# Performance work log

Hardware: AMD Instinct MI355X
Metric: run time of the kernel (lower is better)

The kernel has to match this reference:

```python
import jax, jax.numpy as jnp
import numpy as np

B, N, M, K, D, DO = 4, 32768, 8192, 16, 128, 128


def setup_inputs() -> dict:
    key = jax.random.key(0)
    ks = jax.random.split(key, 8)
    return dict(
        xyz=jax.random.normal(ks[0], (B, N, 3), jnp.float32),
        x=jax.random.normal(ks[1], (B, D, N), jnp.float32),
        xyz_center=jax.random.normal(ks[2], (B, M, 3), jnp.float32),
        idx=jax.random.randint(ks[3], (B, M, K), 0, N, jnp.int32),
        alpha=jnp.ones((1,), jnp.float32),
        beta=jnp.ones((1,), jnp.float32),
        norm_radius=jnp.ones((1,), jnp.float32),
        w1=jax.random.normal(ks[4], (K, 3), jnp.float32) * 0.1,
        g1=jnp.ones((K,), jnp.float32),
        b1=jnp.zeros((K,), jnp.float32),
        w2=jax.random.normal(ks[5], (K, 2 * K), jnp.float32) * 0.1,
        g2=jnp.ones((K,), jnp.float32),
        b2=jnp.zeros((K,), jnp.float32),
        w3=jax.random.normal(ks[6], (K, 2 * K), jnp.float32) * 0.1,
        cv_w=jax.random.normal(ks[7], (DO, D, K), jnp.float32) * 0.02,
    )


def _inorm(t, g, b, eps=1e-5):
    # InstanceNorm2d: normalize each (batch, channel) plane over spatial dims (m, k)
    mu = t.mean(axis=(2, 3), keepdims=True)
    var = t.var(axis=(2, 3), keepdims=True)
    return (t - mu) * jax.lax.rsqrt(var + eps) * g[None, :, None, None] + b[None, :, None, None]


def reference(xyz, x, xyz_center, idx, alpha, beta, norm_radius, w1, g1, b1, w2, g2, b2, w3, cv_w):
    k = idx.shape[-1]
    gather = jax.vmap(lambda pts, i: pts[i])  # per-batch gather
    xyz_group = gather(xyz, idx)                      # b m k 3
    x_group = gather(jnp.swapaxes(x, 1, 2), idx)      # b m k d

    pts = xyz_group - xyz_center[:, :, None, :]       # b m k 3
    # dist computed on detached pts (torch .detach())
    dist = jnp.sqrt(jnp.sum(jnp.square(jax.lax.stop_gradient(pts)), -1))  # b m k
    mean_radius = dist.max(-1).mean()
    nr = norm_radius * 0.9 + mean_radius * 0.1        # EMA-updated radius (non-trainable)
    pts = pts / nr

    dw = jax.nn.sigmoid(-alpha * dist + beta)         # b m k
    s = dw.sum(-1, keepdims=True)
    s = s + (s == 0).astype(dw.dtype) + 1e-6
    dw = dw / s * k
    dw4 = dw[:, None, :, :]                           # b 1 m k

    ptsT = jnp.transpose(pts, (0, 3, 1, 2))           # b 3 m k
    mat = jax.nn.relu(_inorm(jnp.einsum('bcmk,oc->bomk', ptsT, w1), g1, b1))
    mp1 = jnp.broadcast_to((mat * dw4).max(-1, keepdims=True), mat.shape)
    mat = jax.nn.relu(_inorm(jnp.einsum('bcmk,oc->bomk', jnp.concatenate([mat, mp1], 1), w2), g2, b2))
    mp2 = jnp.broadcast_to((mat * dw4).max(-1, keepdims=True), mat.shape)
    mat = jax.nn.relu(jnp.einsum('bcmk,oc->bomk', jnp.concatenate([mat, mp2], 1), w3)) * dw4

    out = jnp.einsum('bmkd,bjmk->bdmj', x_group, mat)  # b d m k
    out = jnp.einsum('bdmj,odj->bom', out, cv_w)
    return out
```

## Files before the change

kernel.cpp:

```cpp
#include <hip/hip_runtime.h>
#include <hip/hip_bf16.h>

#define BB 4
#define NN 32768
#define MM 8192
#define KK 16
#define DD 128
#define DOUT 128
#define TT 2048

typedef unsigned short ushortT;
typedef unsigned int uintT;
typedef __attribute__((ext_vector_type(8))) short short8;
typedef __attribute__((ext_vector_type(4))) float f32x4;
typedef __attribute__((ext_vector_type(2))) float f32x2;

__device__ __forceinline__ ushortT f2bf(float f) {
  union { float f; uintT u; } v; v.f = f;
  uintT u = v.u;
  return (ushortT)((u + 0x7FFFu + ((u >> 16) & 1u)) >> 16);
}

#define ST_MAXD 0
#define ST_E1 16
#define ST_A1 160
#define ST_B1 224
#define ST_E2 288
#define ST_A2 416
#define ST_B2 480

__global__ __launch_bounds__(256) void kxT(const float* __restrict__ x, ushortT* __restrict__ xTb) {
  __shared__ float tile[32][33];
  const int b = blockIdx.z;
  const int n0 = blockIdx.x * 32, d0 = blockIdx.y * 32;
  const int tx = threadIdx.x, ty = threadIdx.y;
  const float* xp = x + (size_t)b * DD * NN;
  #pragma unroll
  for (int i = 0; i < 4; i++)
    tile[ty + i * 8][tx] = xp[(size_t)(d0 + ty + i * 8) * NN + n0 + tx];
  __syncthreads();
  ushortT* op = xTb + (size_t)b * NN * DD;
  #pragma unroll
  for (int i = 0; i < 4; i++)
    op[(size_t)(n0 + ty + i * 8) * DD + d0 + tx] = f2bf(tile[tx][ty + i * 8]);
}

__global__ __launch_bounds__(256) void kWb(const float* __restrict__ cw, ushortT* __restrict__ wb) {
  const int i = blockIdx.x * 256 + threadIdx.x;
  wb[i] = f2bf(cw[i]);
}

__global__ __launch_bounds__(256) void kpassA(const float* __restrict__ xyz,
    const float* __restrict__ xyzc, const int* __restrict__ idx,
    const float* __restrict__ w1, float* __restrict__ st, float4* __restrict__ pts4) {
  const int b = blockIdx.y;
  const int tid = threadIdx.x;
  const int mloc = tid >> 4, k = tid & 15;
  const int m = blockIdx.x * 16 + mloc;
  const int gi = (b * MM + m) * KK + k;
  const int n = idx[gi];
  const float cx = xyzc[(b * MM + m) * 3 + 0];
  const float cy = xyzc[(b * MM + m) * 3 + 1];
  const float cz = xyzc[(b * MM + m) * 3 + 2];
  const float* p = xyz + ((size_t)b * NN + n) * 3;
  const float px = p[0] - cx, py = p[1] - cy, pz = p[2] - cz;
  const float dist = sqrtf(px * px + py * py + pz * pz);
  pts4[gi] = (float4){px, py, pz, dist};
  float maxd = dist;
  maxd = fmaxf(maxd, __shfl_xor(maxd, 1));
  maxd = fmaxf(maxd, __shfl_xor(maxd, 2));
  maxd = fmaxf(maxd, __shfl_xor(maxd, 4));
  maxd = fmaxf(maxd, __shfl_xor(maxd, 8));
  __shared__ float red[16];
  __shared__ float wred[4][32];
  if (k == 0) red[mloc] = maxd;
  float vs[16], vq[16];
  #pragma unroll
  for (int o = 0; o < 16; o++) {
    float e = px * w1[3 * o] + py * w1[3 * o + 1] + pz * w1[3 * o + 2];
    vs[o] = e; vq[o] = e * e;
  }
  #pragma unroll
  for (int s = 1; s < 64; s <<= 1) {
    #pragma unroll
    for (int o = 0; o < 16; o++) {
      vs[o] += __shfl_xor(vs[o], s);
      vq[o] += __shfl_xor(vq[o], s);
    }
  }
  const int wv = tid >> 6, lane = tid & 63;
  if (lane == 0) {
    #pragma unroll
    for (int o = 0; o < 16; o++) { wred[wv][o] = vs[o]; wred[wv][16 + o] = vq[o]; }
  }
  __syncthreads();
  if (tid < 32) {
    float a = wred[0][tid] + wred[1][tid] + wred[2][tid] + wred[3][tid];
    atomicAdd(&st[ST_E1 + b * 32 + tid], a);
  }
  if (tid == 0) {
    float s = 0.f;
    #pragma unroll
    for (int i = 0; i < 16; i++) s += red[i];
    atomicAdd(&st[ST_MAXD], s);
  }
}

__global__ void kS1(const float* __restrict__ nrad, const float* __restrict__ g1,
                    const float* __restrict__ b1, float* __restrict__ st) {
  const int tid = threadIdx.x;
  if (tid >= 64) return;
  const float meanrad = st[ST_MAXD] / (float)(BB * MM);
  const float nr = nrad[0] * 0.9f + meanrad * 0.1f;
  const int b = tid >> 4, o = tid & 15;
  const float cnt = (float)(MM * KK);
  const float sum = st[ST_E1 + b * 32 + o];
  const float sq  = st[ST_E1 + b * 32 + 16 + o];
  const float mu = sum / cnt;
  float var = sq / cnt - mu * mu; var = fmaxf(var, 0.f);
  const float invs = rsqrtf(var + 1e-5f * nr * nr);
  const float a = invs * g1[o];
  st[ST_A1 + b * 16 + o] = a;
  st[ST_B1 + b * 16 + o] = b1[o] - mu * a;
}

__global__ __launch_bounds__(256) void kpassB(const float4* __restrict__ pts4,
    const float* __restrict__ alpha, const float* __restrict__ beta,
    const float* __restrict__ w1, const float* __restrict__ w2,
    float* __restrict__ st) {
  const int b = blockIdx.y;
  const int tid = threadIdx.x;
  __shared__ float wred[4][32];
  const int gi = b * MM * KK + blockIdx.x * 256 + tid;
  const float4 p4 = pts4[gi];
  const float px = p4.x, py = p4.y, pz = p4.z, dist = p4.w;
  float dwv = 1.f / (1.f + expf(alpha[0] * dist - beta[0]));
  float s = dwv;
  s += __shfl_xor(s, 1); s += __shfl_xor(s, 2); s += __shfl_xor(s, 4); s += __shfl_xor(s, 8);
  s = s + (s == 0.f ? 1.f : 0.f) + 1e-6f;
  dwv = dwv / s * 16.f;
  f32x2 v1[16];
  #pragma unroll
  for (int o = 0; o < 16; o++) {
    float e = px * w1[3 * o] + py * w1[3 * o + 1] + pz * w1[3 * o + 2];
    float v = e * st[ST_A1 + b * 16 + o] + st[ST_B1 + b * 16 + o];
    v = fmaxf(v, 0.f);
    float t = v * dwv;
    t = fmaxf(t, __shfl_xor(t, 1)); t = fmaxf(t, __shfl_xor(t, 2));
    t = fmaxf(t, __shfl_xor(t, 4)); t = fmaxf(t, __shfl_xor(t, 8));
    if (o & 1) { v1[o >> 1].y = v; v1[8 + (o >> 1)].y = t; }
    else       { v1[o >> 1].x = v; v1[8 + (o >> 1)].x = t; }
  }
  float vs[16], vq[16];
  #pragma unroll
  for (int o = 0; o < 16; o++) {
    f32x2 acc = {0.f, 0.f};
    #pragma unroll
    for (int cp = 0; cp < 16; cp++) {
      const f32x2 wv = *(const f32x2*)(w2 + o * 32 + 2 * cp);
      acc += v1[cp] * wv;
    }
    const float e = acc.x + acc.y;
    vs[o] = e; vq[o] = e * e;
  }
  #pragma unroll
  for (int s2 = 1; s2 < 64; s2 <<= 1) {
    #pragma unroll
    for (int o = 0; o < 16; o++) {
      vs[o] += __shfl_xor(vs[o], s2);
      vq[o] += __shfl_xor(vq[o], s2);
    }
  }
  const int wv = tid >> 6, lane = tid & 63;
  if (lane == 0) {
    #pragma unroll
    for (int o = 0; o < 16; o++) { wred[wv][o] = vs[o]; wred[wv][16 + o] = vq[o]; }
  }
  __syncthreads();
  if (tid < 32) {
    float a = wred[0][tid] + wred[1][tid] + wred[2][tid] + wred[3][tid];
    atomicAdd(&st[ST_E2 + b * 32 + tid], a);
  }
}

__global__ void kS2(const float* __restrict__ g2, const float* __restrict__ b2,
                    float* __restrict__ st) {
  const int tid = threadIdx.x;
  if (tid >= 64) return;
  const int b = tid >> 4, o = tid & 15;
  const float cnt = (float)(MM * KK);
  const float sum = st[ST_E2 + b * 32 + o];
  const float sq  = st[ST_E2 + b * 32 + 16 + o];
  const float mu = sum / cnt;
  float var = sq / cnt - mu * mu; var = fmaxf(var, 0.f);
  const float invs = rsqrtf(var + 1e-5f);
  const float a = invs * g2[o];
  st[ST_A2 + b * 16 + o] = a;
  st[ST_B2 + b * 16 + o] = b2[o] - mu * a;
}

__global__ __launch_bounds__(256, 6) void kMat3(const float* __restrict__ xyz,
    const float* __restrict__ xyzc, const int* __restrict__ idx,
    const float* __restrict__ alpha, const float* __restrict__ beta,
    const float* __restrict__ w1, const float* __restrict__ w2,
    const float* __restrict__ w3, const float* __restrict__ st,
    float* __restrict__ mat3g) {
  const int b = blockIdx.y;
  const int tid = threadIdx.x;
  const int mloc = tid >> 4, k1 = tid & 15;
  const int m = blockIdx.x * 16 + mloc;
  const int gi = (b * MM + m) * KK + k1;
  const int n = idx[gi];
  const float cx = xyzc[(b * MM + m) * 3 + 0];
  const float cy = xyzc[(b * MM + m) * 3 + 1];
  const float cz = xyzc[(b * MM + m) * 3 + 2];
  const float* p = xyz + ((size_t)b * NN + n) * 3;
  const float px = p[0] - cx, py = p[1] - cy, pz = p[2] - cz;
  const float dist = sqrtf(px * px + py * py + pz * pz);
  float dwv = 1.f / (1.f + expf(alpha[0] * dist - beta[0]));
  {
    float s = dwv;
    s += __shfl_xor(s, 1); s += __shfl_xor(s, 2); s += __shfl_xor(s, 4); s += __shfl_xor(s, 8);
    s = s + (s == 0.f ? 1.f : 0.f) + 1e-6f;
    dwv = dwv / s * 16.f;
  }
  f32x2 v1[16];
  #pragma unroll
  for (int o = 0; o < 16; o++) {
    float e = px * w1[3 * o] + py * w1[3 * o + 1] + pz * w1[3 * o + 2];
    float v = e * st[ST_A1 + b * 16 + o] + st[ST_B1 + b * 16 + o];
    v = fmaxf(v, 0.f);
    float t = v * dwv;
    t = fmaxf(t, __shfl_xor(t, 1)); t = fmaxf(t, __shfl_xor(t, 2));
    t = fmaxf(t, __shfl_xor(t, 4)); t = fmaxf(t, __shfl_xor(t, 8));
    if (o & 1) { v1[o >> 1].y = v; v1[8 + (o >> 1)].y = t; }
    else       { v1[o >> 1].x = v; v1[8 + (o >> 1)].x = t; }
  }
  float in2[16];
  #pragma unroll
  for (int o = 0; o < 16; o++) {
    f32x2 acc = {0.f, 0.f};
    #pragma unroll
    for (int cp = 0; cp < 16; cp++) {
      const f32x2 wv = *(const f32x2*)(w2 + o * 32 + 2 * cp);
      acc += v1[cp] * wv;
    }
    float v = (acc.x + acc.y) * st[ST_A2 + b * 16 + o] + st[ST_B2 + b * 16 + o];
    in2[o] = fmaxf(v, 0.f);
  }
  f32x2 v2[16];
  #pragma unroll
  for (int o = 0; o < 16; o++) {
    float t = in2[o] * dwv;
    t = fmaxf(t, __shfl_xor(t, 1)); t = fmaxf(t, __shfl_xor(t, 2));
    t = fmaxf(t, __shfl_xor(t, 4)); t = fmaxf(t, __shfl_xor(t, 8));
    if (o & 1) { v2[o >> 1].y = in2[o]; v2[8 + (o >> 1)].y = t; }
    else       { v2[o >> 1].x = in2[o]; v2[8 + (o >> 1)].x = t; }
  }
  float m3v[16];
  #pragma unroll
  for (int j = 0; j < 16; j++) {
    f32x2 acc = {0.f, 0.f};
    #pragma unroll
    for (int cp = 0; cp < 16; cp++) {
      const f32x2 wv = *(const f32x2*)(w3 + j * 32 + 2 * cp);
      acc += v2[cp] * wv;
    }
    m3v[j] = fmaxf(acc.x + acc.y, 0.f) * dwv;
  }
  const int swz1 = (k1 ^ (k1 >> 2)) & 3;
  float* m3w = mat3g + (((size_t)b * MM + blockIdx.x * 16) << 8) + tid * 16;
  #pragma unroll
  for (int q = 0; q < 4; q++)
    *(f32x4*)(m3w + ((q ^ swz1) << 2)) =
        (f32x4){m3v[4 * q], m3v[4 * q + 1], m3v[4 * q + 2], m3v[4 * q + 3]};
}

__global__ __launch_bounds__(512, 4) void kF2(const int* __restrict__ idx,
    const float* __restrict__ mat3g, const ushortT* __restrict__ xTb,
    ushortT* __restrict__ Aout) {
  __shared__ float mat3s[32 * 256];
  const int b = blockIdx.y;
  const int tid = threadIdx.x;
  const int m0 = blockIdx.x * 32;

  const int wid = __builtin_amdgcn_readfirstlane(tid >> 6);
  const int lane = tid & 63;
  const int jh = lane >> 5;
  const int dq = lane & 31;
  const int d0 = dq * 4;
  const int jq0 = jh * 2;
  const ushortT* xb = xTb + (size_t)b * NN * DD + d0;

  uint2 xA[16], xB[16];

#define PREF(dst, gg) do {                                                 \
    const int* ib = idx + (((b * MM + m0 + (gg) * 8 + wid)) << 4);         \
    _Pragma("unroll")                                                      \
    for (int k = 0; k < 16; k++) {                                         \
      const uintT nn = (uintT)ib[k];                                       \
      (dst)[k] = *(const uint2*)(xb + ((size_t)nn << 7));                  \
    }                                                                      \
  } while (0)

  PREF(xA, 0);

  {
    const float* src = mat3g + (((size_t)b * MM + m0) << 8) + tid * 16;
    float* dst = &mat3s[tid * 16];
    #pragma unroll
    for (int q = 0; q < 4; q++)
      *(f32x4*)(dst + q * 4) = *(const f32x4*)(src + q * 4);
  }
  __syncthreads();

#define COMP(src, gg) do {                                                 \
    const int ml = (gg) * 8 + wid;                                         \
    const float* m3base = &mat3s[ml * 256];                                \
    f32x2 a2[4][4];                                                        \
    _Pragma("unroll")                                                      \
    for (int d = 0; d < 4; d++)                                            \
      _Pragma("unroll")                                                    \
      for (int c = 0; c < 4; c++) a2[d][c] = (f32x2){0.f, 0.f};            \
    _Pragma("unroll")                                                      \
    for (int k = 0; k < 16; k++) {                                         \
      const int sw = (k ^ (k >> 2)) & 3;                                   \
      const uint2 xv = (src)[k];                                           \
      const f32x4 mq0 = *(const f32x4*)(m3base + k * 16 + ((jq0 ^ sw) << 2));        \
      const f32x4 mq1 = *(const f32x4*)(m3base + k * 16 + (((jq0 + 1) ^ sw) << 2));  \
      float xs[4];                                                         \
      xs[0] = __uint_as_float(xv.x << 16);                                 \
      xs[1] = __uint_as_float(xv.x & 0xFFFF0000u);                         \
      xs[2] = __uint_as_float(xv.y << 16);                                 \
      xs[3] = __uint_as_float(xv.y & 0xFFFF0000u);                         \
      f32x2 mp[4];                                                         \
      mp[0] = mq0.lo; mp[1] = mq0.hi;                                      \
      mp[2] = mq1.lo; mp[3] = mq1.hi;                                      \
      _Pragma("unroll")                                                    \
      for (int d = 0; d < 4; d++) {                                        \
        const float xd = xs[d];                                            \
        _Pragma("unroll")                                                  \
        for (int c = 0; c < 4; c++)                                        \
          a2[d][c] += mp[c] * xd;                                          \
      }                                                                    \
    }                                                                      \
    ushortT* aop = Aout + ((size_t)b * MM + m0 + ml) * TT + d0 * 16 + jh * 8;  \
    _Pragma("unroll")                                                      \
    for (int d = 0; d < 4; d++) {                                          \
      uintT u[4];                                                          \
      _Pragma("unroll")                                                    \
      for (int c = 0; c < 4; c++)                                          \
        u[c] = (uintT)f2bf(a2[d][c].x) | ((uintT)f2bf(a2[d][c].y) << 16);  \
      *(uint4*)(aop + d * 16) = (uint4){u[0], u[1], u[2], u[3]};           \
    }                                                                      \
  } while (0)

  PREF(xB, 1);
  COMP(xA, 0);
  PREF(xA, 2);
  COMP(xB, 1);
  PREF(xB, 3);
  COMP(xA, 2);
  COMP(xB, 3);

#undef PREF
#undef COMP
}

__global__ __launch_bounds__(512) void kgemm(const ushortT* __restrict__ Wb,
                                             const ushortT* __restrict__ Aout,
                                             float* __restrict__ out) {
  __shared__ ushortT At[128 * 40];
  __shared__ ushortT Bt[128 * 40];
  const int b = blockIdx.y;
  const int m0 = blockIdx.x * 128;
  const int tid = threadIdx.x;
  const int w = tid >> 6, l = tid & 63;
  const int ow = (w >> 2) * 64, mw = (w & 3) * 32;
  const int fr = l & 15, fg = l >> 4;
  f32x4 acc[4][2];
  #pragma unroll
  for (int i = 0; i < 4; i++)
    #pragma unroll
    for (int j = 0; j < 2; j++)
      acc[i][j] = (f32x4){0.f, 0.f, 0.f, 0.f};
  const int srow = tid >> 2, sk = (tid & 3) * 8;
  const ushortT* wp = Wb + srow * TT + sk;
  const ushortT* ap = Aout + ((size_t)b * MM + m0 + srow) * TT + sk;
  for (int k0 = 0; k0 < TT; k0 += 32) {
    uint4 wv = *(const uint4*)(wp + k0);
    uint4 av = *(const uint4*)(ap + k0);
    *(uint4*)&At[srow * 40 + sk] = wv;
    *(uint4*)&Bt[srow * 40 + sk] = av;
    __syncthreads();
    short8 a[4], bfrag[2];
    #pragma unroll
    for (int i = 0; i < 4; i++) a[i] = *(short8*)&At[(ow + i * 16 + fr) * 40 + fg * 8];
    #pragma unroll
    for (int j = 0; j < 2; j++) bfrag[j] = *(short8*)&Bt[(mw + j * 16 + fr) * 40 + fg * 8];
    #pragma unroll
    for (int i = 0; i < 4; i++)
      #pragma unroll
      for (int j = 0; j < 2; j++)
        acc[i][j] = __builtin_amdgcn_mfma_f32_16x16x32_bf16(a[i], bfrag[j], acc[i][j], 0, 0, 0);
    __syncthreads();
  }
  #pragma unroll
  for (int i = 0; i < 4; i++)
    #pragma unroll
    for (int j = 0; j < 2; j++)
      #pragma unroll
      for (int r = 0; r < 4; r++) {
        const int o = ow + i * 16 + fg * 4 + r;
        const int m = m0 + mw + j * 16 + fr;
        out[((size_t)b * DOUT + o) * MM + m] = acc[i][j][r];
      }
}

#define XTB_OFF 0
#define PTS_OFF 33554432
#define MAT3_OFF 33554432
#define AOUT_OFF 67108864
#define WB_OFF 201326592
#define ST_OFF 201850880

extern "C" void kernel_launch(void* const* d_in, const int* in_sizes, int n_in,
                              void* d_out, int out_size, void* d_ws, size_t ws_size,
                              hipStream_t stream) {
  const float* xyz  = (const float*)d_in[0];
  const float* x    = (const float*)d_in[1];
  const float* xyzc = (const float*)d_in[2];
  const int*   idx  = (const int*)d_in[3];
  const float* alpha = (const float*)d_in[4];
  const float* beta  = (const float*)d_in[5];
  const float* nrad  = (const float*)d_in[6];
  const float* w1 = (const float*)d_in[7];
  const float* g1 = (const float*)d_in[8];
  const float* b1 = (const float*)d_in[9];
  const float* w2 = (const float*)d_in[10];
  const float* g2 = (const float*)d_in[11];
  const float* b2 = (const float*)d_in[12];
  const float* w3 = (const float*)d_in[13];
  const float* cvw = (const float*)d_in[14];
  char* ws = (char*)d_ws;
  ushortT* xTb  = (ushortT*)(ws + XTB_OFF);
  float4*  pts4 = (float4*)(ws + PTS_OFF);
  float*   mat3g = (float*)(ws + MAT3_OFF);
  ushortT* Aout = (ushortT*)(ws + AOUT_OFF);
  ushortT* Wb   = (ushortT*)(ws + WB_OFF);
  float*   st   = (float*)(ws + ST_OFF);
  float* out = (float*)d_out;

  hipMemsetAsync(st, 0, 4096, stream);
  kxT<<<dim3(NN / 32, DD / 32, BB), dim3(32, 8), 0, stream>>>(x, xTb);
  kWb<<<dim3(DOUT * TT / 256), 256, 0, stream>>>(cvw, Wb);
  kpassA<<<dim3(MM / 16, BB), 256, 0, stream>>>(xyz, xyzc, idx, w1, st, pts4);
  kS1<<<1, 64, 0, stream>>>(nrad, g1, b1, st);
  kpassB<<<dim3(MM / 16, BB), 256, 0, stream>>>(pts4, alpha, beta, w1, w2, st);
  kS2<<<1, 64, 0, stream>>>(g2, b2, st);
  kMat3<<<dim3(MM / 16, BB), 256, 0, stream>>>(xyz, xyzc, idx, alpha, beta, w1, w2, w3, st, mat3g);
  kF2<<<dim3(MM / 32, BB), 512, 0, stream>>>(idx, mat3g, xTb, Aout);
  kgemm<<<dim3(MM / 128, BB), 512, 0, stream>>>(Wb, Aout, out);
}
```

Before: 222.7 us.

## Remap kF2 lanes so each half-wave computes all 16 outputs of one point

In kF2 each half-wave now handles a separate center point and computes all 16 j outputs, where before the two half-waves split the j outputs of a single point. Each gathered x row is therefore loaded once per point instead of twice, which halves the gather traffic and cuts the four prefetch/compute stages to two. The shared-memory staging of mat3 switches to coalesced strided f32x4 copies. In exchange there are twice as many accumulators per thread, and launch bounds drop from 4 to 3 waves, which lowers occupancy.

```diff
diff --git a/kernel.cpp b/kernel.cpp
--- a/kernel.cpp
+++ b/kernel.cpp
@@ -276,7 +276,7 @@
         (f32x4){m3v[4 * q], m3v[4 * q + 1], m3v[4 * q + 2], m3v[4 * q + 3]};
 }
 
-__global__ __launch_bounds__(512, 4) void kF2(const int* __restrict__ idx,
+__global__ __launch_bounds__(512, 3) void kF2(const int* __restrict__ idx,
     const float* __restrict__ mat3g, const ushortT* __restrict__ xTb,
     ushortT* __restrict__ Aout) {
   __shared__ float mat3s[32 * 256];
@@ -286,82 +286,83 @@
 
   const int wid = __builtin_amdgcn_readfirstlane(tid >> 6);
   const int lane = tid & 63;
-  const int jh = lane >> 5;
+  const int mh = lane >> 5;
   const int dq = lane & 31;
   const int d0 = dq * 4;
-  const int jq0 = jh * 2;
   const ushortT* xb = xTb + (size_t)b * NN * DD + d0;
 
   uint2 xA[16], xB[16];
 
 #define PREF(dst, gg) do {                                                 \
-    const int* ib = idx + (((b * MM + m0 + (gg) * 8 + wid)) << 4);         \
+    const int* ib0 = idx + ((b * MM + m0 + (gg) * 16 + wid * 2) << 4);     \
+    const int* ib1 = ib0 + 16;                                             \
     _Pragma("unroll")                                                      \
-    for (int k = 0; k < 16; k++) {                                         \
-      const uintT nn = (uintT)ib[k];                                       \
-      (dst)[k] = *(const uint2*)(xb + ((size_t)nn << 7));                  \
+    for (int t = 0; t < 16; t++) {                                         \
+      const int ke = ib0[t], ko = ib1[t];                                  \
+      const uintT nn = (uintT)(mh ? ko : ke);                              \
+      (dst)[t] = *(const uint2*)(xb + ((size_t)nn << 7));                  \
     }                                                                      \
   } while (0)
 
   PREF(xA, 0);
 
   {
-    const float* src = mat3g + (((size_t)b * MM + m0) << 8) + tid * 16;
-    float* dst = &mat3s[tid * 16];
-    #pragma unroll
-    for (int q = 0; q < 4; q++)
-      *(f32x4*)(dst + q * 4) = *(const f32x4*)(src + q * 4);
+    const f32x4* src = (const f32x4*)(mat3g + (((size_t)b * MM + m0) << 8));
+    f32x4* dst = (f32x4*)mat3s;
+    #pragma unroll
+    for (int i = 0; i < 4; i++)
+      dst[tid + i * 512] = src[tid + i * 512];
   }
   __syncthreads();
 
 #define COMP(src, gg) do {                                                 \
-    const int ml = (gg) * 8 + wid;                                         \
-    const float* m3base = &mat3s[ml * 256];                                \
-    f32x2 a2[4][4];                                                        \
+    const float* m3base = &mat3s[((gg) * 16 + wid * 2 + mh) * 256];        \
+    f32x2 a2[4][8];                                                        \
     _Pragma("unroll")                                                      \
     for (int d = 0; d < 4; d++)                                            \
       _Pragma("unroll")                                                    \
-      for (int c = 0; c < 4; c++) a2[d][c] = (f32x2){0.f, 0.f};            \
+      for (int c = 0; c < 8; c++) a2[d][c] = (f32x2){0.f, 0.f};            \
     _Pragma("unroll")                                                      \
-    for (int k = 0; k < 16; k++) {                                         \
-      const int sw = (k ^ (k >> 2)) & 3;                                   \
-      const uint2 xv = (src)[k];                                           \
-      const f32x4 mq0 = *(const f32x4*)(m3base + k * 16 + ((jq0 ^ sw) << 2));        \
-      const f32x4 mq1 = *(const f32x4*)(m3base + k * 16 + (((jq0 + 1) ^ sw) << 2));  \
+    for (int t = 0; t < 16; t++) {                                         \
+      const int sw = (t ^ (t >> 2)) & 3;                                   \
+      const uint2 xv = (src)[t];                                           \
+      const f32x4 mq0 = *(const f32x4*)(m3base + t * 16 + ((0 ^ sw) << 2));\
+      const f32x4 mq1 = *(const f32x4*)(m3base + t * 16 + ((1 ^ sw) << 2));\
+      const f32x4 mq2 = *(const f32x4*)(m3base + t * 16 + ((2 ^ sw) << 2));\
+      const f32x4 mq3 = *(const f32x4*)(m3base + t * 16 + ((3 ^ sw) << 2));\
       float xs[4];                                                         \
       xs[0] = __uint_as_float(xv.x << 16);                                 \
       xs[1] = __uint_as_float(xv.x & 0xFFFF0000u);                         \
       xs[2] = __uint_as_float(xv.y << 16);                                 \
       xs[3] = __uint_as_float(xv.y & 0xFFFF0000u);                         \
-      f32x2 mp[4];                                                         \
+      f32x2 mp[8];                                                         \
       mp[0] = mq0.lo; mp[1] = mq0.hi;                                      \
       mp[2] = mq1.lo; mp[3] = mq1.hi;                                      \
+      mp[4] = mq2.lo; mp[5] = mq2.hi;                                      \
+      mp[6] = mq3.lo; mp[7] = mq3.hi;                                      \
       _Pragma("unroll")                                                    \
       for (int d = 0; d < 4; d++) {                                        \
         const float xd = xs[d];                                            \
         _Pragma("unroll")                                                  \
-        for (int c = 0; c < 4; c++)                                        \
+        for (int c = 0; c < 8; c++)                                        \
           a2[d][c] += mp[c] * xd;                                          \
       }                                                                    \
     }                                                                      \
-    ushortT* aop = Aout + ((size_t)b * MM + m0 + ml) * TT + d0 * 16 + jh * 8;  \
+    ushortT* aop = Aout + ((size_t)b * MM + m0 + (gg) * 16 + wid * 2 + mh) * TT + d0 * 16; \
     _Pragma("unroll")                                                      \
     for (int d = 0; d < 4; d++) {                                          \
-      uintT u[4];                                                          \
+      uintT u[8];                                                          \
       _Pragma("unroll")                                                    \
-      for (int c = 0; c < 4; c++)                                          \
+      for (int c = 0; c < 8; c++)                                          \
         u[c] = (uintT)f2bf(a2[d][c].x) | ((uintT)f2bf(a2[d][c].y) << 16);  \
-      *(uint4*)(aop + d * 16) = (uint4){u[0], u[1], u[2], u[3]};           \
+      *(uint4*)(aop + d * 16)     = (uint4){u[0], u[1], u[2], u[3]};       \
+      *(uint4*)(aop + d * 16 + 8) = (uint4){u[4], u[5], u[6], u[7]};       \
     }                                                                      \
   } while (0)
 
   PREF(xB, 1);
   COMP(xA, 0);
-  PREF(xA, 2);
   COMP(xB, 1);
-  PREF(xB, 3);
-  COMP(xA, 2);
-  COMP(xB, 3);
 
 #undef PREF
 #undef COMP
```

Result: slower. 236.2 us (+6.1%).
